# Optimization experiments

Measured on AMD Instinct MI355X. Metric: run time of the kernel, lower is better.

## Reference

```python
import jax, jax.numpy as jnp
import numpy as np
from jax import lax

KERNEL_SIZES = (3, 5, 7)
EPS = 1e-12  # torch F.normalize default eps


def _gamma(x, k):
    """SpatialCorrelationSampler(kernel_size=k)(x, F.normalize(x, dim=1)).

    With patch_size=1, stride=1, padding=0, dilation=1 the sampler output at
    (b, y, x) is sum over channels and the kxk window of in1 * in2. Since
    in2 = in1 / max(||in1||_c, eps), the channel contraction collapses to
    ||x||^2 / max(||x||, eps) per pixel, followed by a kxk box-sum (VALID).
    x: [B, C, H, W] -> gamma: [B, H-k+1, W-k+1]
    """
    norm = jnp.sqrt(jnp.sum(x * x, axis=1))          # [B, H, W]
    p = (norm * norm) / jnp.maximum(norm, EPS)       # [B, H, W]
    return lax.reduce_window(p, 0.0, lax.add, (1, k, k), (1, 1, 1), 'VALID')


def reference(out_feat0, out_feat1, gt_feat0, gt_feat1):
    loss = jnp.float32(0.0)
    for xo, xg in ((out_feat0, gt_feat0), (out_feat1, gt_feat1)):
        for k in KERNEL_SIZES:
            go = _gamma(xo, k)
            gg = _gamma(xg, k)
            loss = loss + jnp.mean((go - gg) ** 2)   # nn.MSELoss (mean)
    return loss


def setup_inputs() -> dict:
    key = jax.random.key(0)
    k0, k1, k2, k3 = jax.random.split(key, 4)
    return {
        'out_feat0': jax.random.normal(k0, (8, 256, 64, 64), dtype=jnp.float32),
        'out_feat1': jax.random.normal(k1, (8, 512, 32, 32), dtype=jnp.float32),
        'gt_feat0': jax.random.normal(k2, (8, 256, 64, 64), dtype=jnp.float32),
        'gt_feat1': jax.random.normal(k3, (8, 512, 32, 32), dtype=jnp.float32),
    }
```

## Files before the change

### kernel.cpp

```cpp
#include <hip/hip_runtime.h>
#include <math.h>

#define EPS 1e-12f

template <int W, int C, int H>
__device__ __forceinline__ void norm_diff_row(
    const float* __restrict__ xo, const float* __restrict__ xg,
    float* __restrict__ d, int bh, int tid, float* lds )
{
    constexpr int QUADS  = W / 4;
    constexpr int CCHUNK = 256 / QUADS;
    constexpr int CPT    = C / CCHUNK;
    static_assert(2 * CCHUNK * W == 2048, "lds size");

    const int quad = tid % QUADS;
    const int cgrp = tid / QUADS;
    const int b    = bh / H;
    const int h    = bh % H;

    const int plane = H * W;
    const int base  = b * C * plane + h * W + quad * 4;
    const int c0    = cgrp * CPT;

    float4 so = make_float4(0.f, 0.f, 0.f, 0.f);
    float4 sg = make_float4(0.f, 0.f, 0.f, 0.f);
#pragma unroll 4
    for (int i = 0; i < CPT; ++i) {
        const int off = base + (c0 + i) * plane;
        const float4 vo = *reinterpret_cast<const float4*>(xo + off);
        const float4 vg = *reinterpret_cast<const float4*>(xg + off);
        so.x = fmaf(vo.x, vo.x, so.x);
        so.y = fmaf(vo.y, vo.y, so.y);
        so.z = fmaf(vo.z, vo.z, so.z);
        so.w = fmaf(vo.w, vo.w, so.w);
        sg.x = fmaf(vg.x, vg.x, sg.x);
        sg.y = fmaf(vg.y, vg.y, sg.y);
        sg.z = fmaf(vg.z, vg.z, sg.z);
        sg.w = fmaf(vg.w, vg.w, sg.w);
    }

    *reinterpret_cast<float4*>(lds + (0 * CCHUNK + cgrp) * W + quad * 4) = so;
    *reinterpret_cast<float4*>(lds + (1 * CCHUNK + cgrp) * W + quad * 4) = sg;
    __syncthreads();

    if (tid < W) {
        float ao = 0.f, ag = 0.f;
#pragma unroll
        for (int g = 0; g < CCHUNK; ++g) {
            ao += lds[(0 * CCHUNK + g) * W + tid];
            ag += lds[(1 * CCHUNK + g) * W + tid];
        }
        const float no = sqrtf(ao);
        const float ng = sqrtf(ag);
        const float po = ao / fmaxf(no, EPS);
        const float pg = ag / fmaxf(ng, EPS);
        d[bh * W + tid] = po - pg;
    }
}

__global__ __launch_bounds__(256) void stage1_kernel(
    const float* __restrict__ o0, const float* __restrict__ g0,
    const float* __restrict__ o1, const float* __restrict__ g1,
    float* __restrict__ d0, float* __restrict__ d1,
    float* __restrict__ out)
{
    __shared__ float lds[2048];
    const int bid = blockIdx.x;
    if (bid == 0 && threadIdx.x == 0) out[0] = 0.0f;
    if (bid < 8 * 64) {
        norm_diff_row<64, 256, 64>(o0, g0, d0, bid, threadIdx.x, lds);
    } else {
        norm_diff_row<32, 512, 32>(o1, g1, d1, bid - 8 * 64, threadIdx.x, lds);
    }
}

__global__ __launch_bounds__(256) void boxmse_kernel(
    const float* __restrict__ d0, const float* __restrict__ d1,
    float* __restrict__ out)
{
    __shared__ float img[64 * 64];
    __shared__ float rows[64 * 64];
    __shared__ float wsum[4];

    const int bid = blockIdx.x;
    const int t   = bid / 24;
    const int rem = bid % 24;
    const int b   = rem / 3;
    const int ki  = rem % 3;
    const int k   = 3 + 2 * ki;
    const int H   = (t == 0) ? 64 : 32;
    const float* src = ((t == 0) ? d0 : d1) + b * H * H;

    const int tid = threadIdx.x;
    const int N   = H * H;
    for (int i = tid; i < N; i += 256) img[i] = src[i];
    __syncthreads();

    const int V = H - k + 1;

    for (int i = tid; i < H * V; i += 256) {
        const int h = i / V;
        const int w = i - h * V;
        float s = 0.f;
        for (int j = 0; j < k; ++j) s += img[h * H + w + j];
        rows[h * V + w] = s;
    }
    __syncthreads();

    float acc = 0.f;
    for (int i = tid; i < V * V; i += 256) {
        const int y = i / V;
        const int x = i - y * V;
        float s = 0.f;
        for (int j = 0; j < k; ++j) s += rows[(y + j) * V + x];
        acc = fmaf(s, s, acc);
    }

    for (int off = 32; off > 0; off >>= 1) acc += __shfl_down(acc, off);
    if ((tid & 63) == 0) wsum[tid >> 6] = acc;
    __syncthreads();
    if (tid == 0) {
        const float total = wsum[0] + wsum[1] + wsum[2] + wsum[3];
        const float inv_count = 1.0f / (float)(8 * V * V);
        atomicAdd(out, total * inv_count);
    }
}

extern "C" void kernel_launch(void* const* d_in, const int* in_sizes, int n_in,
                              void* d_out, int out_size, void* d_ws, size_t ws_size,
                              hipStream_t stream) {
    const float* out_feat0 = (const float*)d_in[0];
    const float* out_feat1 = (const float*)d_in[1];
    const float* gt_feat0  = (const float*)d_in[2];
    const float* gt_feat1  = (const float*)d_in[3];
    float* out = (float*)d_out;

    float* d0 = (float*)d_ws;
    float* d1 = d0 + 8 * 64 * 64;

    stage1_kernel<<<8 * 64 + 8 * 32, 256, 0, stream>>>(
        out_feat0, gt_feat0, out_feat1, gt_feat1, d0, d1, out);
    boxmse_kernel<<<48, 256, 0, stream>>>(d0, d1, out);
}
```

Baseline: 130.9 us.

## Fuse horizontal box-sum into stage1 and use nontemporal vector loads

```diff
diff --git a/kernel.cpp b/kernel.cpp
--- a/kernel.cpp
+++ b/kernel.cpp
@@ -3,15 +3,18 @@
 
 #define EPS 1e-12f
 
+typedef float f4 __attribute__((ext_vector_type(4)));
+
 template <int W, int C, int H>
-__device__ __forceinline__ void norm_diff_row(
+__device__ __forceinline__ void row_kernel(
     const float* __restrict__ xo, const float* __restrict__ xg,
-    float* __restrict__ d, int bh, int tid, float* lds )
+    float* __restrict__ r,
+    int bh, int tid, float* lds , float* drow )
 {
     constexpr int QUADS  = W / 4;
     constexpr int CCHUNK = 256 / QUADS;
     constexpr int CPT    = C / CCHUNK;
-    static_assert(2 * CCHUNK * W == 2048, "lds size");
+    constexpr int NR     = 8 * H;
 
     const int quad = tid % QUADS;
     const int cgrp = tid / QUADS;
@@ -22,25 +25,19 @@
     const int base  = b * C * plane + h * W + quad * 4;
     const int c0    = cgrp * CPT;
 
-    float4 so = make_float4(0.f, 0.f, 0.f, 0.f);
-    float4 sg = make_float4(0.f, 0.f, 0.f, 0.f);
+    f4 so = {0.f, 0.f, 0.f, 0.f};
+    f4 sg = {0.f, 0.f, 0.f, 0.f};
 #pragma unroll 4
     for (int i = 0; i < CPT; ++i) {
         const int off = base + (c0 + i) * plane;
-        const float4 vo = *reinterpret_cast<const float4*>(xo + off);
-        const float4 vg = *reinterpret_cast<const float4*>(xg + off);
-        so.x = fmaf(vo.x, vo.x, so.x);
-        so.y = fmaf(vo.y, vo.y, so.y);
-        so.z = fmaf(vo.z, vo.z, so.z);
-        so.w = fmaf(vo.w, vo.w, so.w);
-        sg.x = fmaf(vg.x, vg.x, sg.x);
-        sg.y = fmaf(vg.y, vg.y, sg.y);
-        sg.z = fmaf(vg.z, vg.z, sg.z);
-        sg.w = fmaf(vg.w, vg.w, sg.w);
+        const f4 vo = __builtin_nontemporal_load(reinterpret_cast<const f4*>(xo + off));
+        const f4 vg = __builtin_nontemporal_load(reinterpret_cast<const f4*>(xg + off));
+        so += vo * vo;
+        sg += vg * vg;
     }
 
-    *reinterpret_cast<float4*>(lds + (0 * CCHUNK + cgrp) * W + quad * 4) = so;
-    *reinterpret_cast<float4*>(lds + (1 * CCHUNK + cgrp) * W + quad * 4) = sg;
+    *reinterpret_cast<f4*>(lds + (0 * CCHUNK + cgrp) * W + quad * 4) = so;
+    *reinterpret_cast<f4*>(lds + (1 * CCHUNK + cgrp) * W + quad * 4) = sg;
     __syncthreads();
 
     if (tid < W) {
@@ -54,32 +51,46 @@
         const float ng = sqrtf(ag);
         const float po = ao / fmaxf(no, EPS);
         const float pg = ag / fmaxf(ng, EPS);
-        d[bh * W + tid] = po - pg;
+        drow[tid] = po - pg;
+    }
+    __syncthreads();
+
+#pragma unroll
+    for (int ki = 0; ki < 3; ++ki) {
+        const int k = 3 + 2 * ki;
+        const int V = W - k + 1;
+        if (tid < V) {
+            float s = 0.f;
+#pragma unroll
+            for (int j = 0; j < 7; ++j)
+                if (j < k) s += drow[tid + j];
+            r[(ki * NR + bh) * W + tid] = s;
+        }
     }
 }
 
 __global__ __launch_bounds__(256) void stage1_kernel(
     const float* __restrict__ o0, const float* __restrict__ g0,
     const float* __restrict__ o1, const float* __restrict__ g1,
-    float* __restrict__ d0, float* __restrict__ d1,
+    float* __restrict__ r0, float* __restrict__ r1,
     float* __restrict__ out)
 {
     __shared__ float lds[2048];
+    __shared__ float drow[64];
     const int bid = blockIdx.x;
     if (bid == 0 && threadIdx.x == 0) out[0] = 0.0f;
     if (bid < 8 * 64) {
-        norm_diff_row<64, 256, 64>(o0, g0, d0, bid, threadIdx.x, lds);
+        row_kernel<64, 256, 64>(o0, g0, r0, bid, threadIdx.x, lds, drow);
     } else {
-        norm_diff_row<32, 512, 32>(o1, g1, d1, bid - 8 * 64, threadIdx.x, lds);
+        row_kernel<32, 512, 32>(o1, g1, r1, bid - 8 * 64, threadIdx.x, lds, drow);
     }
 }
 
 __global__ __launch_bounds__(256) void boxmse_kernel(
-    const float* __restrict__ d0, const float* __restrict__ d1,
+    const float* __restrict__ r0, const float* __restrict__ r1,
     float* __restrict__ out)
 {
-    __shared__ float img[64 * 64];
-    __shared__ float rows[64 * 64];
+    __shared__ float img[64 * 62];
     __shared__ float wsum[4];
 
     const int bid = blockIdx.x;
@@ -89,21 +100,15 @@
     const int ki  = rem % 3;
     const int k   = 3 + 2 * ki;
     const int H   = (t == 0) ? 64 : 32;
-    const float* src = ((t == 0) ? d0 : d1) + b * H * H;
+    const int V   = H - k + 1;
+    const float* src = ((t == 0) ? r0 : r1) + (ki * (8 * H) + b * H) * H;
 
     const int tid = threadIdx.x;
-    const int N   = H * H;
-    for (int i = tid; i < N; i += 256) img[i] = src[i];
-    __syncthreads();
-
-    const int V = H - k + 1;
 
     for (int i = tid; i < H * V; i += 256) {
-        const int h = i / V;
-        const int w = i - h * V;
-        float s = 0.f;
-        for (int j = 0; j < k; ++j) s += img[h * H + w + j];
-        rows[h * V + w] = s;
+        const int y = i / V;
+        const int x = i - y * V;
+        img[i] = src[y * H + x];
     }
     __syncthreads();
 
@@ -112,7 +117,7 @@
         const int y = i / V;
         const int x = i - y * V;
         float s = 0.f;
-        for (int j = 0; j < k; ++j) s += rows[(y + j) * V + x];
+        for (int j = 0; j < k; ++j) s += img[(y + j) * V + x];
         acc = fmaf(s, s, acc);
     }
 
@@ -135,10 +140,10 @@
     const float* gt_feat1  = (const float*)d_in[3];
     float* out = (float*)d_out;
 
-    float* d0 = (float*)d_ws;
-    float* d1 = d0 + 8 * 64 * 64;
+    float* r0 = (float*)d_ws;
+    float* r1 = r0 + 3 * 512 * 64;
 
     stage1_kernel<<<8 * 64 + 8 * 32, 256, 0, stream>>>(
-        out_feat0, gt_feat0, out_feat1, gt_feat1, d0, d1, out);
-    boxmse_kernel<<<48, 256, 0, stream>>>(d0, d1, out);
+        out_feat0, gt_feat0, out_feat1, gt_feat1, r0, r1, out);
+    boxmse_kernel<<<48, 256, 0, stream>>>(r0, r1, out);
 }
```

After: 128.7 us, median of 2. Within noise of the previous version (-1.7%).
